# Optimization experiments

Hardware: AMD Instinct MI355X
Metric: run time of the kernel (lower is better)

Reference implementation:

```python
import jax, jax.numpy as jnp
from jax import lax
import numpy as np

OUT_SCALE = 0.001
DN = ('NCHW', 'OIHW', 'NCHW')


def _dw_res_gelu(v, w, b):
    # depthwise 3x3 conv (groups = C) + bias, residual add, exact GELU (torch nn.GELU default)
    y = lax.conv_general_dilated(v, w, (1, 1), ((1, 1), (1, 1)),
                                 feature_group_count=v.shape[1],
                                 dimension_numbers=DN)
    y = y + b[None, :, None, None]
    return jax.nn.gelu(v + y, approximate=False)


def setup_inputs() -> dict:
    key = jax.random.key(0)
    ks = jax.random.split(key, 6)
    B, C = 64, 64
    return {
        'z': jax.random.normal(ks[0], (B, C, 16, 16), jnp.float32),
        'x': jax.random.normal(ks[1], (B, C, 96, 96), jnp.float32),
        'wz': jax.random.normal(ks[2], (C, 1, 3, 3), jnp.float32) * 0.1,
        'bz': jax.random.normal(ks[3], (C,), jnp.float32) * 0.1,
        'wx': jax.random.normal(ks[4], (C, 1, 3, 3), jnp.float32) * 0.1,
        'bx': jax.random.normal(ks[5], (C,), jnp.float32) * 0.1,
    }


def reference(z, x, wz, bz, wx, bx):
    x = _dw_res_gelu(x, wx, bx)
    z = _dw_res_gelu(z, wz, bz)
    B, C, zh, zw = z.shape
    nx, _, h, w = x.shape
    # fast batched cross-correlation: view search as one image with B*C channels,
    # use templates z as [O=B, I=C, zh, zw] filters with feature_group_count=B
    xr = x.reshape(1, nx * C, h, w)
    out = lax.conv_general_dilated(xr, z, (1, 1),
                                   ((zh // 2, zh // 2), (zw // 2, zw // 2)),
                                   feature_group_count=B,
                                   dimension_numbers=DN)
    out = out.reshape(nx, -1, out.shape[-2], out.shape[-1])
    return out * OUT_SCALE
```

## Files before the change

### kernel.cpp

```cpp
#include <hip/hip_runtime.h>
#include <hip/hip_bf16.h>

typedef unsigned short ushortT;
typedef __bf16 bf16x8 __attribute__((ext_vector_type(8)));
typedef float f32x4 __attribute__((ext_vector_type(4)));

#define OUT_SCALE 0.001f

__device__ __forceinline__ float gelu_fast(float v) {
    const float u = v * fmaf(0.044715f * v, v, 1.0f);
    const float e = __expf(-1.5957691216057308f * u);
    return v * __builtin_amdgcn_rcpf(1.0f + e);
}
__device__ __forceinline__ ushortT f2bf(float f) {
    __hip_bfloat16 h = __float2bfloat16(f);
    return *reinterpret_cast<ushortT*>(&h);
}

__global__ __launch_bounds__(256) void k_gelu_z(
    const float* __restrict__ z, const float* __restrict__ wz,
    const float* __restrict__ bz, ushortT* __restrict__ zbuf)
{
    const int b  = blockIdx.x;
    const int cg = blockIdx.y;
    const int tid = threadIdx.x;

    __shared__ float zs[16 * 260];

    for (int i = tid; i < 1024; i += 256) {
        const int c_l = i >> 6, pos = i & 63;
        *(float4*)(zs + c_l * 260 + pos * 4) =
            *(const float4*)(z + ((size_t)(b * 64 + cg * 16 + c_l)) * 256 + pos * 4);
    }
    __syncthreads();

    const int c_l = tid & 15;
    const int v   = tid >> 4;
    const int c   = cg * 16 + c_l;

    float w[9];
    #pragma unroll
    for (int i = 0; i < 9; ++i) w[i] = wz[c * 9 + i];
    const float bias = bz[c];
    const float* zc = zs + c_l * 260;
    ushortT* zo = zbuf + (size_t)b * 16384 + c;

    #pragma unroll
    for (int u = 0; u < 16; ++u) {
        float acc = bias;
        #pragma unroll
        for (int dr = 0; dr < 3; ++dr) {
            const int uu = u + dr - 1;
            if (uu < 0 || uu >= 16) continue;
            #pragma unroll
            for (int dc = 0; dc < 3; ++dc) {
                const int vv = v + dc - 1;
                if (vv < 0 || vv >= 16) continue;
                acc += zc[uu * 16 + vv] * w[dr * 3 + dc];
            }
        }
        const float y = acc + zc[u * 16 + v];
        zo[(v * 16 + u) * 64] = f2bf(gelu_fast(y));
    }
}

__global__ __launch_bounds__(512, 4) void k_fused(
    const float* __restrict__ x, const float* __restrict__ wx,
    const float* __restrict__ bx, const ushortT* __restrict__ zbuf,
    float* __restrict__ part)
{
    const int lin = blockIdx.x;
    const int sw  = ((lin & 7) * 384) + (lin >> 3);
    const int k2  = sw % 48;
    const int b   = sw / 48;
    const int r0  = k2 * 2;
    const int tid = threadIdx.x;

    __shared__ ushortT rowbuf[2][8192];

    {
        const int row = tid >> 8, g = (tid >> 7) & 1, t = tid & 127;
        const int off = (t < 32) ? t * 8 : 3328 + (t - 32) * 8;
        *(uint4*)(&rowbuf[row][g * 4096 + off]) = make_uint4(0, 0, 0, 0);
    }

    {
        const int c = tid >> 3, colg = tid & 7, j0 = colg * 12;
        const int g_ = c >> 5, cl = c & 31, chunk = cl >> 3, pos = cl & 7;

        float w[9];
        #pragma unroll
        for (int i = 0; i < 9; ++i) w[i] = wx[c * 9 + i];
        const float bias = bx[c];
        const float* xb = x + (size_t)(b * 64 + c) * 9216;

        float acc0[12], acc1[12];
        #pragma unroll
        for (int jj = 0; jj < 12; ++jj) { acc0[jj] = bias; acc1[jj] = bias; }

        #pragma unroll
        for (int s = 0; s < 4; ++s) {
            const int rr  = r0 - 1 + s;
            const int rcl = (rr < 0) ? 0 : (rr > 95 ? 95 : rr);
            const bool rok = (rr >= 0) && (rr < 96);
            float f[20];
            #pragma unroll
            for (int m = 0; m < 5; ++m) {
                const int cs  = j0 - 4 + 4 * m;
                const int csc = (cs < 0) ? 0 : (cs > 92 ? 92 : cs);
                const float4 v = *(const float4*)(xb + rcl * 96 + csc);
                const bool ok = rok && (cs >= 0) && (cs <= 92);
                f[4 * m + 0] = ok ? v.x : 0.f;
                f[4 * m + 1] = ok ? v.y : 0.f;
                f[4 * m + 2] = ok ? v.z : 0.f;
                f[4 * m + 3] = ok ? v.w : 0.f;
            }
            if (s == 0) {
                #pragma unroll
                for (int jj = 0; jj < 12; ++jj)
                    acc0[jj] += f[jj+3]*w[0] + f[jj+4]*w[1] + f[jj+5]*w[2];
            } else if (s == 1) {
                #pragma unroll
                for (int jj = 0; jj < 12; ++jj) {
                    acc0[jj] += f[jj+3]*w[3] + f[jj+4]*w[4] + f[jj+5]*w[5]
                              + f[jj+4];
                    acc1[jj] += f[jj+3]*w[0] + f[jj+4]*w[1] + f[jj+5]*w[2];
                }
            } else if (s == 2) {
                #pragma unroll
                for (int jj = 0; jj < 12; ++jj) {
                    acc0[jj] += f[jj+3]*w[6] + f[jj+4]*w[7] + f[jj+5]*w[8];
                    acc1[jj] += f[jj+3]*w[3] + f[jj+4]*w[4] + f[jj+5]*w[5]
                              + f[jj+4];
                }
            } else {
                #pragma unroll
                for (int jj = 0; jj < 12; ++jj)
                    acc1[jj] += f[jj+3]*w[6] + f[jj+4]*w[7] + f[jj+5]*w[8];
            }
        }

        ushortT* rbw0 = &rowbuf[0][0] + g_ * 4096;
        ushortT* rbw1 = &rowbuf[1][0] + g_ * 4096;
        #pragma unroll
        for (int jj = 0; jj < 12; ++jj) {
            const int T  = j0 + jj + 8;
            const int sh = T * 32 + ((chunk ^ ((T >> 1) & 3)) << 3) + pos;
            rbw0[sh] = f2bf(gelu_fast(acc0[jj]));
            rbw1[sh] = f2bf(gelu_fast(acc1[jj]));
        }
    }
    __syncthreads();

    const int wave = tid >> 6;
    const int lane = tid & 63;
    const int n    = lane & 15;
    const int q    = lane >> 4;
    if (wave < 7) {
        const int j0a = wave * 16;
        const ushortT* zb = zbuf + (size_t)b * 16384;
        f32x4 acc0 = {0.f, 0.f, 0.f, 0.f};
        f32x4 acc1 = {0.f, 0.f, 0.f, 0.f};

        #pragma unroll
        for (int g = 0; g < 2; ++g) {
            bf16x8 bfrag[16];
            #pragma unroll
            for (int v = 0; v < 16; ++v)
                bfrag[v] = *(const bf16x8*)(zb + (v * 16 + n) * 64 + g * 32 + 8 * q);
            #pragma unroll
            for (int v = 0; v < 16; ++v) {
                const int T = j0a + n + v;
                const int off = (g * 128 + T) * 32 + ((q ^ ((T >> 1) & 3)) << 3);
                const bf16x8 a0 = *(const bf16x8*)(&rowbuf[0][0] + off);
                acc0 = __builtin_amdgcn_mfma_f32_16x16x32_bf16(a0, bfrag[v], acc0, 0, 0, 0);
                const bf16x8 a1 = *(const bf16x8*)(&rowbuf[1][0] + off);
                acc1 = __builtin_amdgcn_mfma_f32_16x16x32_bf16(a1, bfrag[v], acc1, 0, 0, 0);
            }
        }

        const int ii = 15 - n;
        const int joff = j0a + 4 * q;
        f32x4* p0 = (f32x4*)(part + ((size_t)(b * 96 + r0) * 16 + ii) * 112 + joff);
        *p0 = acc0;
        f32x4* p1 = (f32x4*)(part + ((size_t)(b * 96 + r0 + 1) * 16 + ii) * 112 + joff);
        *p1 = acc1;
    }
}

__global__ __launch_bounds__(256) void k_reduce(
    const float* __restrict__ part, float* __restrict__ out)
{
    const int gid = blockIdx.x * 256 + threadIdx.x;
    if (gid >= 64 * 97 * 25) return;
    const int j4 = gid % 25;
    const int t  = gid / 25;
    const int i  = t % 97;
    const int b  = t / 97;
    const int j  = j4 * 4;

    int rlo = i - 8;  if (rlo < 0)  rlo = 0;
    int rhi = i + 7;  if (rhi > 95) rhi = 95;

    const float* p = part + ((size_t)(b * 96 + rlo) * 16 + (i - rlo + 7)) * 112 + j;
    f32x4 s = {0.f, 0.f, 0.f, 0.f};
    for (int r = rlo; r <= rhi; ++r) {
        s += *(const f32x4*)p;
        p += 1680;
    }
    float* ob = out + (size_t)b * 9409 + i * 97 + j;
    ob[0] = s[0] * OUT_SCALE;
    if (j < 96) {
        ob[1] = s[1] * OUT_SCALE;
        ob[2] = s[2] * OUT_SCALE;
        ob[3] = s[3] * OUT_SCALE;
    }
}

extern "C" void kernel_launch(void* const* d_in, const int* in_sizes, int n_in,
                              void* d_out, int out_size, void* d_ws, size_t ws_size,
                              hipStream_t stream)
{
    const float* z  = (const float*)d_in[0];
    const float* x  = (const float*)d_in[1];
    const float* wz = (const float*)d_in[2];
    const float* bz = (const float*)d_in[3];
    const float* wx = (const float*)d_in[4];
    const float* bx = (const float*)d_in[5];
    float* out = (float*)d_out;

    ushortT* zbuf = (ushortT*)d_ws;
    float*   partw = (float*)((char*)d_ws + (size_t)64 * 16384 * 2);

    k_gelu_z<<<dim3(64, 4), 256, 0, stream>>>(z, wz, bz, zbuf);
    k_fused<<<dim3(3072), 512, 0, stream>>>(x, wx, bx, zbuf, partw);
    const int nred = 64 * 97 * 25;
    k_reduce<<<dim3((nred + 255) / 256), 256, 0, stream>>>(partw, out);

    (void)in_sizes; (void)n_in; (void)ws_size; (void)out_size;
}
```

Baseline: 324.7 us.

## Process six rows per block with rolling register window and double-buffered LDS

Each block now handles six output rows instead of two, keeping a rolling three-row register window of input so each x row is loaded once rather than twice per pair. The next row's global loads are issued before the MFMA stage and its depthwise conv plus GELU is written into the alternate LDS buffer, overlapping memory traffic with matrix work. The grid drops from 3072 to 1024 blocks. This cuts redundant halo loads and launch count but adds a syncthreads per row and more register pressure, with fewer blocks available for occupancy.

```diff
diff --git a/kernel.cpp b/kernel.cpp
--- a/kernel.cpp
+++ b/kernel.cpp
@@ -70,121 +70,131 @@
     float* __restrict__ part)
 {
     const int lin = blockIdx.x;
-    const int sw  = ((lin & 7) * 384) + (lin >> 3);
-    const int k2  = sw % 48;
-    const int b   = sw / 48;
-    const int r0  = k2 * 2;
+    const int sw  = ((lin & 7) << 7) + (lin >> 3);
+    const int b   = sw >> 4;
+    const int r0  = (sw & 15) * 6;
     const int tid = threadIdx.x;
 
     __shared__ ushortT rowbuf[2][8192];
 
     {
-        const int row = tid >> 8, g = (tid >> 7) & 1, t = tid & 127;
+        const int bu = tid >> 8, g = (tid >> 7) & 1, t = tid & 127;
         const int off = (t < 32) ? t * 8 : 3328 + (t - 32) * 8;
-        *(uint4*)(&rowbuf[row][g * 4096 + off]) = make_uint4(0, 0, 0, 0);
+        *(uint4*)(&rowbuf[bu][g * 4096 + off]) = make_uint4(0, 0, 0, 0);
+    }
+
+    const int c = tid >> 3, colg = tid & 7, j0 = colg * 12;
+    const int g_ = c >> 5, cl = c & 31, chunk = cl >> 3, pos = cl & 7;
+    const int wave = tid >> 6, lane = tid & 63;
+    const int n = lane & 15, q = lane >> 4, j0a = wave * 16;
+    const bool ledge = (colg == 0), redge = (colg == 7);
+
+    float w[9];
+    #pragma unroll
+    for (int i = 0; i < 9; ++i) w[i] = wx[c * 9 + i];
+    const float bias = bx[c];
+    const float* xb = x + (size_t)(b * 64 + c) * 9216;
+    const ushortT* zb = zbuf + (size_t)b * 16384;
+
+    float W[3][20];
+
+    #pragma unroll
+    for (int s = 0; s < 3; ++s) {
+        const int rr  = r0 - 1 + s;
+        const int rcl = (rr < 0) ? 0 : rr;
+        const bool rok = (rr >= 0);
+        const float* xr = xb + rcl * 96;
+        #pragma unroll
+        for (int m = 0; m < 5; ++m) {
+            const int cs  = j0 - 4 + 4 * m;
+            const int csc = (cs < 0) ? 0 : (cs > 92 ? 92 : cs);
+            const float4 v = *(const float4*)(xr + csc);
+            const bool ok = rok && !(m == 0 && ledge) && !(m == 4 && redge);
+            W[s][4*m+0] = ok ? v.x : 0.f;
+            W[s][4*m+1] = ok ? v.y : 0.f;
+            W[s][4*m+2] = ok ? v.z : 0.f;
+            W[s][4*m+3] = ok ? v.w : 0.f;
+        }
     }
 
     {
-        const int c = tid >> 3, colg = tid & 7, j0 = colg * 12;
-        const int g_ = c >> 5, cl = c & 31, chunk = cl >> 3, pos = cl & 7;
-
-        float w[9];
+        ushortT* rbw = &rowbuf[0][0] + g_ * 4096;
         #pragma unroll
-        for (int i = 0; i < 9; ++i) w[i] = wx[c * 9 + i];
-        const float bias = bx[c];
-        const float* xb = x + (size_t)(b * 64 + c) * 9216;
-
-        float acc0[12], acc1[12];
-        #pragma unroll
-        for (int jj = 0; jj < 12; ++jj) { acc0[jj] = bias; acc1[jj] = bias; }
-
-        #pragma unroll
-        for (int s = 0; s < 4; ++s) {
-            const int rr  = r0 - 1 + s;
-            const int rcl = (rr < 0) ? 0 : (rr > 95 ? 95 : rr);
-            const bool rok = (rr >= 0) && (rr < 96);
-            float f[20];
+        for (int jj = 0; jj < 12; ++jj) {
+            const float a = bias
+              + W[0][jj+3]*w[0] + W[0][jj+4]*w[1] + W[0][jj+5]*w[2]
+              + W[1][jj+3]*w[3] + W[1][jj+4]*w[4] + W[1][jj+5]*w[5] + W[1][jj+4]
+              + W[2][jj+3]*w[6] + W[2][jj+4]*w[7] + W[2][jj+5]*w[8];
+            const int T = j0 + jj + 8;
+            rbw[T*32 + ((chunk ^ ((T>>1)&3)) << 3) + pos] = f2bf(gelu_fast(a));
+        }
+    }
+    __syncthreads();
+
+    #pragma unroll
+    for (int it = 0; it < 6; ++it) {
+        float4 raw[5];
+        bool rok = false;
+        if (it < 5) {
+            const int rr  = r0 + it + 2;
+            const int rcl = (rr > 95) ? 95 : rr;
+            rok = (rr <= 95);
+            const float* xr = xb + rcl * 96;
             #pragma unroll
             for (int m = 0; m < 5; ++m) {
                 const int cs  = j0 - 4 + 4 * m;
                 const int csc = (cs < 0) ? 0 : (cs > 92 ? 92 : cs);
-                const float4 v = *(const float4*)(xb + rcl * 96 + csc);
-                const bool ok = rok && (cs >= 0) && (cs <= 92);
-                f[4 * m + 0] = ok ? v.x : 0.f;
-                f[4 * m + 1] = ok ? v.y : 0.f;
-                f[4 * m + 2] = ok ? v.z : 0.f;
-                f[4 * m + 3] = ok ? v.w : 0.f;
-            }
-            if (s == 0) {
+                raw[m] = *(const float4*)(xr + csc);
+            }
+        }
+        __builtin_amdgcn_sched_barrier(0);
+
+        if (wave < 7) {
+            const ushortT* rb = &rowbuf[it & 1][0];
+            f32x4 acc = {0.f, 0.f, 0.f, 0.f};
+            #pragma unroll
+            for (int g = 0; g < 2; ++g) {
+                bf16x8 bf[16];
                 #pragma unroll
-                for (int jj = 0; jj < 12; ++jj)
-                    acc0[jj] += f[jj+3]*w[0] + f[jj+4]*w[1] + f[jj+5]*w[2];
-            } else if (s == 1) {
+                for (int v = 0; v < 16; ++v)
+                    bf[v] = *(const bf16x8*)(zb + (v*16 + n)*64 + g*32 + 8*q);
                 #pragma unroll
-                for (int jj = 0; jj < 12; ++jj) {
-                    acc0[jj] += f[jj+3]*w[3] + f[jj+4]*w[4] + f[jj+5]*w[5]
-                              + f[jj+4];
-                    acc1[jj] += f[jj+3]*w[0] + f[jj+4]*w[1] + f[jj+5]*w[2];
+                for (int v = 0; v < 16; ++v) {
+                    const int T = j0a + n + v;
+                    const int off = (g*128 + T)*32 + ((q ^ ((T>>1)&3)) << 3);
+                    const bf16x8 a = *(const bf16x8*)(rb + off);
+                    acc = __builtin_amdgcn_mfma_f32_16x16x32_bf16(a, bf[v], acc, 0, 0, 0);
                 }
-            } else if (s == 2) {
-                #pragma unroll
-                for (int jj = 0; jj < 12; ++jj) {
-                    acc0[jj] += f[jj+3]*w[6] + f[jj+4]*w[7] + f[jj+5]*w[8];
-                    acc1[jj] += f[jj+3]*w[3] + f[jj+4]*w[4] + f[jj+5]*w[5]
-                              + f[jj+4];
-                }
-            } else {
-                #pragma unroll
-                for (int jj = 0; jj < 12; ++jj)
-                    acc1[jj] += f[jj+3]*w[6] + f[jj+4]*w[7] + f[jj+5]*w[8];
-            }
-        }
-
-        ushortT* rbw0 = &rowbuf[0][0] + g_ * 4096;
-        ushortT* rbw1 = &rowbuf[1][0] + g_ * 4096;
-        #pragma unroll
-        for (int jj = 0; jj < 12; ++jj) {
-            const int T  = j0 + jj + 8;
-            const int sh = T * 32 + ((chunk ^ ((T >> 1) & 3)) << 3) + pos;
-            rbw0[sh] = f2bf(gelu_fast(acc0[jj]));
-            rbw1[sh] = f2bf(gelu_fast(acc1[jj]));
-        }
-    }
-    __syncthreads();
-
-    const int wave = tid >> 6;
-    const int lane = tid & 63;
-    const int n    = lane & 15;
-    const int q    = lane >> 4;
-    if (wave < 7) {
-        const int j0a = wave * 16;
-        const ushortT* zb = zbuf + (size_t)b * 16384;
-        f32x4 acc0 = {0.f, 0.f, 0.f, 0.f};
-        f32x4 acc1 = {0.f, 0.f, 0.f, 0.f};
-
-        #pragma unroll
-        for (int g = 0; g < 2; ++g) {
-            bf16x8 bfrag[16];
-            #pragma unroll
-            for (int v = 0; v < 16; ++v)
-                bfrag[v] = *(const bf16x8*)(zb + (v * 16 + n) * 64 + g * 32 + 8 * q);
-            #pragma unroll
-            for (int v = 0; v < 16; ++v) {
-                const int T = j0a + n + v;
-                const int off = (g * 128 + T) * 32 + ((q ^ ((T >> 1) & 3)) << 3);
-                const bf16x8 a0 = *(const bf16x8*)(&rowbuf[0][0] + off);
-                acc0 = __builtin_amdgcn_mfma_f32_16x16x32_bf16(a0, bfrag[v], acc0, 0, 0, 0);
-                const bf16x8 a1 = *(const bf16x8*)(&rowbuf[1][0] + off);
-                acc1 = __builtin_amdgcn_mfma_f32_16x16x32_bf16(a1, bfrag[v], acc1, 0, 0, 0);
-            }
-        }
-
-        const int ii = 15 - n;
-        const int joff = j0a + 4 * q;
-        f32x4* p0 = (f32x4*)(part + ((size_t)(b * 96 + r0) * 16 + ii) * 112 + joff);
-        *p0 = acc0;
-        f32x4* p1 = (f32x4*)(part + ((size_t)(b * 96 + r0 + 1) * 16 + ii) * 112 + joff);
-        *p1 = acc1;
+            }
+            const int ii = 15 - n;
+            *(f32x4*)(part + ((size_t)(b*96 + r0 + it)*16 + ii)*112 + j0a + 4*q) = acc;
+        }
+
+        if (it < 5) {
+            float* Wn = W[it % 3];
+            #pragma unroll
+            for (int m = 0; m < 5; ++m) {
+                const bool ok = rok && !(m == 0 && ledge) && !(m == 4 && redge);
+                Wn[4*m+0] = ok ? raw[m].x : 0.f;
+                Wn[4*m+1] = ok ? raw[m].y : 0.f;
+                Wn[4*m+2] = ok ? raw[m].z : 0.f;
+                Wn[4*m+3] = ok ? raw[m].w : 0.f;
+            }
+            const float* fm1 = W[(it + 1) % 3];
+            const float* fc  = W[(it + 2) % 3];
+            const float* fp1 = Wn;
+            ushortT* rbw = &rowbuf[(it + 1) & 1][0] + g_ * 4096;
+            #pragma unroll
+            for (int jj = 0; jj < 12; ++jj) {
+                const float a = bias
+                  + fm1[jj+3]*w[0] + fm1[jj+4]*w[1] + fm1[jj+5]*w[2]
+                  + fc [jj+3]*w[3] + fc [jj+4]*w[4] + fc [jj+5]*w[5] + fc[jj+4]
+                  + fp1[jj+3]*w[6] + fp1[jj+4]*w[7] + fp1[jj+5]*w[8];
+                const int T = j0 + jj + 8;
+                rbw[T*32 + ((chunk ^ ((T>>1)&3)) << 3) + pos] = f2bf(gelu_fast(a));
+            }
+            __syncthreads();
+        }
     }
 }
 
@@ -233,7 +243,7 @@
     float*   partw = (float*)((char*)d_ws + (size_t)64 * 16384 * 2);
 
     k_gelu_z<<<dim3(64, 4), 256, 0, stream>>>(z, wz, bz, zbuf);
-    k_fused<<<dim3(3072), 512, 0, stream>>>(x, wx, bx, zbuf, partw);
+    k_fused<<<dim3(1024), 512, 0, stream>>>(x, wx, bx, zbuf, partw);
     const int nred = 64 * 97 * 25;
     k_reduce<<<dim3((nred + 255) / 256), 256, 0, stream>>>(partw, out);
 
```

Result: slower. 521.4 us (+60.6%).
